# Optimization experiments

Measured on AMD Instinct MI355X. Metric: run time of the kernel, lower is better.

Reference implementation:

```python
import jax, jax.numpy as jnp
import numpy as np

N_DET, N_MAP, N_PTS, C = 900, 100, 20, 256
IMG_W, IMG_H = 640.0, 480.0


def _grid_sample(feat, gx, gy):
    """Bilinear grid_sample, align_corners=False, zeros padding.
    feat: [C,H,W]; gx,gy: [N] normalized in [-1,1]. Returns [N,C]."""
    Cc, H, W = feat.shape
    x = (gx + 1.0) * (W * 0.5) - 0.5
    y = (gy + 1.0) * (H * 0.5) - 0.5
    x0 = jnp.floor(x); y0 = jnp.floor(y)
    wx1 = x - x0; wx0 = 1.0 - wx1
    wy1 = y - y0; wy0 = 1.0 - wy1

    def gather(xi, yi):
        inb = (xi >= 0) & (xi <= W - 1) & (yi >= 0) & (yi <= H - 1)
        xc = jnp.clip(xi, 0, W - 1).astype(jnp.int32)
        yc = jnp.clip(yi, 0, H - 1).astype(jnp.int32)
        return feat[:, yc, xc] * inb.astype(feat.dtype)  # [C,N]

    out = (gather(x0, y0) * (wx0 * wy0) + gather(x0 + 1, y0) * (wx1 * wy0)
           + gather(x0, y0 + 1) * (wx0 * wy1) + gather(x0 + 1, y0 + 1) * (wx1 * wy1))
    return out.T  # [N,C]


def _project(E, K, homo):
    """E:[6,4,4], K:[6,3,3], homo:[N,4] -> gx,gy,valid each [6,N]."""
    pc = jnp.einsum('cij,nj->cni', E, homo)            # [6,N,4]
    p2d = jnp.einsum('cij,cnj->cni', K, pc[..., :3])   # [6,N,3]
    depth = p2d[..., 2]
    u = p2d[..., 0] / (depth + 1e-6)
    v = p2d[..., 1] / (depth + 1e-6)
    valid = depth > 0.1
    gx = u / IMG_W * 2.0 - 1.0
    gy = v / IMG_H * 2.0 - 1.0
    return gx, gy, valid


def _sample_multiscale(feats, gx, gy, valid):
    """feats: list of [6,C,H,W]; gx,gy,valid: [6,N] -> [6,N,C]."""
    acc = None
    for f in feats:  # fixed 4 FPN levels
        s = jax.vmap(_grid_sample)(f, gx, gy)  # [6,N,C]
        acc = s if acc is None else acc + s
    acc = acc / len(feats)
    return acc * valid[..., None].astype(acc.dtype)


def setup_inputs():
    key = jax.random.key(0)
    ks = jax.random.split(key, 16)
    f = lambda i, shape, s=1.0: jax.random.normal(ks[i], shape, jnp.float32) * s
    p2 = f(0, (6, C, 120, 160))
    p3 = f(1, (6, C, 60, 80))
    p4 = f(2, (6, C, 30, 40))
    p5 = f(3, (6, C, 15, 20))
    K0 = jnp.array([[500.0, 0.0, 320.0], [0.0, 500.0, 240.0], [0.0, 0.0, 1.0]], jnp.float32)
    intrinsics = jnp.tile(K0, (6, 1, 1)) + f(4, (6, 3, 3), 0.5)
    extrinsics = jnp.tile(jnp.eye(4, dtype=jnp.float32), (6, 1, 1)) + f(5, (6, 4, 4), 0.3)
    det_anchors_3d = f(6, (N_DET, 3), 20.0)
    det_anchors_full = f(7, (N_DET, 11))
    map_anchors = f(8, (N_MAP, N_PTS, 2), 20.0)
    s = 1.0 / float(np.sqrt(C))
    return {
        'p2': p2, 'p3': p3, 'p4': p4, 'p5': p5,
        'intrinsics': intrinsics, 'extrinsics': extrinsics,
        'det_anchors_3d': det_anchors_3d, 'det_anchors_full': det_anchors_full,
        'map_anchors': map_anchors,
        'W1d': f(9, (C, C), s), 'b1d': jnp.zeros((C,), jnp.float32),
        'Wcd': f(10, (C, 4), s), 'bcd': jnp.zeros((4,), jnp.float32),
        'Wod': f(11, (C, 11), s), 'bod': jnp.zeros((11,), jnp.float32),
        'W1m': f(12, (C, C), s), 'b1m': jnp.zeros((C,), jnp.float32),
        'Wcm': f(13, (C, 3), s), 'bcm': jnp.zeros((3,), jnp.float32),
        'Wom': f(14, (C, N_PTS * 2), s), 'bom': jnp.zeros((N_PTS * 2,), jnp.float32),
    }


def reference(p2, p3, p4, p5, intrinsics, extrinsics, det_anchors_3d,
              det_anchors_full, map_anchors, W1d, b1d, Wcd, bcd, Wod, bod,
              W1m, b1m, Wcm, bcm, Wom, bom):
    feats = [p2, p3, p4, p5]
    ones_det = jnp.ones((N_DET, 1), det_anchors_3d.dtype)
    homo_det = jnp.concatenate([det_anchors_3d, ones_det], axis=-1)  # [900,4]
    centers = map_anchors.mean(axis=1)  # [100,2]
    homo_map = jnp.concatenate([centers,
                                jnp.zeros((N_MAP, 1), centers.dtype),
                                jnp.ones((N_MAP, 1), centers.dtype)], axis=-1)  # [100,4]

    gxd, gyd, vd = _project(extrinsics, intrinsics, homo_det)
    det_agg = _sample_multiscale(feats, gxd, gyd, vd).sum(0) / 6.0  # [900,256]
    gxm, gym, vm = _project(extrinsics, intrinsics, homo_map)
    map_agg = _sample_multiscale(feats, gxm, gym, vm).sum(0) / 6.0  # [100,256]

    hd = jax.nn.relu(det_agg @ W1d + b1d)
    det_classes = hd @ Wcd + bcd                     # [900,4]
    det_boxes = det_anchors_full + hd @ Wod + bod    # [900,11]
    hm = jax.nn.relu(map_agg @ W1m + b1m)
    map_classes = hm @ Wcm + bcm                     # [100,3]
    map_lines = map_anchors + (hm @ Wom + bom).reshape(N_MAP, N_PTS, 2)
    return det_classes, det_boxes, map_classes, map_lines
```

## Files before the change

### kernel.cpp

```cpp
#include <hip/hip_runtime.h>

#define CDIM 256
#define NDET 900
#define NMAP 100
#define NPTS 20
#define NBLK (NDET + NMAP)

using u16 = unsigned short;

#define U4OFF 7372800
#define U5OFF 9216000
#define UEND  9676800
#define ACCF  4838400
#define C3STR 1228800
#define C4STR 307200
#define C5STR 76800

__device__ __forceinline__ u16 f2bf(float f) {
    union { float f; unsigned int i; } v; v.f = f;
    return (u16)((v.i + 0x7FFFu + ((v.i >> 16) & 1u)) >> 16);
}
__device__ __forceinline__ float bf2f(u16 u) {
    union { unsigned int i; float f; } v; v.i = ((unsigned int)u) << 16; return v.f;
}

__global__ __launch_bounds__(256, 4) void k1_pack_p2(
    const float* __restrict__ p2, const float* __restrict__ p3,
    const float* __restrict__ p4, const float* __restrict__ p5,
    const float* __restrict__ Kin, const float* __restrict__ Ein,
    const float* __restrict__ det3d, const float* __restrict__ mapanch,
    u16* __restrict__ wsb, float* __restrict__ accw)
{
    const int b = blockIdx.x;
    const int t = threadIdx.x;

    __shared__ float s_tile[64][65];

    if (b < 1800) {
        const int cam = b / 300;
        const int rem = b % 300;
        const int pxT = rem >> 2, chT = rem & 3;
        const int lane = t & 63, wv = t >> 6;
        #pragma unroll
        for (int cc = 0; cc < 16; ++cc) {
            const int chl = wv * 16 + cc;
            s_tile[chl][lane] = p3[(cam * CDIM + chT * 64 + chl) * 4800 + pxT * 64 + lane];
        }
        __syncthreads();
        #pragma unroll
        for (int pp = 0; pp < 16; ++pp) {
            const int pxl = wv * 16 + pp;
            wsb[(cam * 4800 + pxT * 64 + pxl) * CDIM + chT * 64 + lane] = f2bf(s_tile[lane][pxl]);
        }
        return;
    }
    if (b < 1980) {
        const int id = b - 1800;
        const int cam = id / 30, h = id % 30;
        const float4* __restrict__ src = (const float4*)(p4 + ((cam * CDIM + t) * 30 + h) * 40);
        u16* __restrict__ dst = wsb + U4OFF + ((cam * 30 + h) * 40) * CDIM + t;
        #pragma unroll
        for (int w4 = 0; w4 < 10; ++w4) {
            const float4 v = src[w4];
            dst[(w4 * 4 + 0) * CDIM] = f2bf(v.x);
            dst[(w4 * 4 + 1) * CDIM] = f2bf(v.y);
            dst[(w4 * 4 + 2) * CDIM] = f2bf(v.z);
            dst[(w4 * 4 + 3) * CDIM] = f2bf(v.w);
        }
        return;
    }
    if (b < 2070) {
        const int id = b - 1980;
        const int cam = id / 15, h = id % 15;
        const float4* __restrict__ src = (const float4*)(p5 + ((cam * CDIM + t) * 15 + h) * 20);
        u16* __restrict__ dst = wsb + U5OFF + ((cam * 15 + h) * 20) * CDIM + t;
        #pragma unroll
        for (int w4 = 0; w4 < 5; ++w4) {
            const float4 v = src[w4];
            dst[(w4 * 4 + 0) * CDIM] = f2bf(v.x);
            dst[(w4 * 4 + 1) * CDIM] = f2bf(v.y);
            dst[(w4 * 4 + 2) * CDIM] = f2bf(v.z);
            dst[(w4 * 4 + 3) * CDIM] = f2bf(v.w);
        }
        return;
    }

    const int pt = b - 2070;
    const bool isDet = (pt < NDET);
    const int m = pt - NDET;

    __shared__ int   s_off0[7][4];
    __shared__ float s_w0[7][4];
    __shared__ int   s_list0[8];
    __shared__ int   s_n0;

    if (t < 7) {
        float h0, h1, h2;
        if (isDet) {
            h0 = det3d[pt * 3 + 0];
            h1 = det3d[pt * 3 + 1];
            h2 = det3d[pt * 3 + 2];
        } else {
            float cx = 0.f, cy = 0.f;
            #pragma unroll
            for (int j = 0; j < NPTS; ++j) {
                cx += mapanch[(m * NPTS + j) * 2 + 0];
                cy += mapanch[(m * NPTS + j) * 2 + 1];
            }
            h0 = cx / (float)NPTS; h1 = cy / (float)NPTS; h2 = 0.f;
        }
        bool pred = false;
        if (t < 6) {
            const int cam = t;
            float pc[3];
            #pragma unroll
            for (int i = 0; i < 3; ++i) {
                pc[i] = Ein[cam * 16 + i * 4 + 0] * h0
                      + Ein[cam * 16 + i * 4 + 1] * h1
                      + Ein[cam * 16 + i * 4 + 2] * h2
                      + Ein[cam * 16 + i * 4 + 3] * 1.f;
            }
            const float q0 = Kin[cam*9+0]*pc[0] + Kin[cam*9+1]*pc[1] + Kin[cam*9+2]*pc[2];
            const float q1 = Kin[cam*9+3]*pc[0] + Kin[cam*9+4]*pc[1] + Kin[cam*9+5]*pc[2];
            const float q2 = Kin[cam*9+6]*pc[0] + Kin[cam*9+7]*pc[1] + Kin[cam*9+8]*pc[2];
            const float depth = q2;
            const float u = q0 / (depth + 1e-6f);
            const float v = q1 / (depth + 1e-6f);
            const bool valid = (depth > 0.1f);
            const float gx = u / 640.0f * 2.0f - 1.0f;
            const float gy = v / 480.0f * 2.0f - 1.0f;
            const int H = 120, W = 160;
            const float x = (gx + 1.f) * (W * 0.5f) - 0.5f;
            const float y = (gy + 1.f) * (H * 0.5f) - 0.5f;
            const float x0f = floorf(x), y0f = floorf(y);
            const float wx1 = x - x0f, wx0 = 1.f - wx1;
            const float wy1 = y - y0f, wy0 = 1.f - wy1;
            const float x1f = x0f + 1.f, y1f = y0f + 1.f;
            const bool bx0 = (x0f >= 0.f) && (x0f <= (float)(W - 1));
            const bool bx1 = (x1f >= 0.f) && (x1f <= (float)(W - 1));
            const bool by0 = (y0f >= 0.f) && (y0f <= (float)(H - 1));
            const bool by1 = (y1f >= 0.f) && (y1f <= (float)(H - 1));
            const int xc0 = (int)fminf(fmaxf(x0f, 0.f), (float)(W - 1));
            const int xc1 = (int)fminf(fmaxf(x1f, 0.f), (float)(W - 1));
            const int yc0 = (int)fminf(fmaxf(y0f, 0.f), (float)(H - 1));
            const int yc1 = (int)fminf(fmaxf(y1f, 0.f), (float)(H - 1));
            const int base = cam * CDIM * H * W;
            s_off0[t][0] = base + yc0 * W + xc0;
            s_off0[t][1] = base + yc0 * W + xc1;
            s_off0[t][2] = base + yc1 * W + xc0;
            s_off0[t][3] = base + yc1 * W + xc1;
            const float w0 = (bx0 && by0) ? wx0 * wy0 : 0.f;
            const float w1 = (bx1 && by0) ? wx1 * wy0 : 0.f;
            const float w2 = (bx0 && by1) ? wx0 * wy1 : 0.f;
            const float w3 = (bx1 && by1) ? wx1 * wy1 : 0.f;
            s_w0[t][0] = w0; s_w0[t][1] = w1; s_w0[t][2] = w2; s_w0[t][3] = w3;
            pred = valid && ((w0 + w1 + w2 + w3) != 0.f);
        } else {
            s_off0[6][0] = 0; s_off0[6][1] = 0; s_off0[6][2] = 0; s_off0[6][3] = 0;
            s_w0[6][0] = 0.f; s_w0[6][1] = 0.f; s_w0[6][2] = 0.f; s_w0[6][3] = 0.f;
        }
        const unsigned long long mask = __ballot(pred);
        const int n = __popcll(mask);
        const int rank = __popcll(mask & ((1ull << t) - 1ull));
        if (pred) s_list0[rank] = t;
        const int npad = (n + 1) & ~1;
        if (t < 2 && (n + t) < npad) s_list0[n + t] = 6;
        if (t == 0) s_n0 = npad;
    }
    __syncthreads();

    float acc = 0.f;
    const int npad = s_n0;
    const int cHW = t * 19200;
    for (int base = 0; base < npad; base += 2) {
        float v[2][4];
        int tj[2];
        #pragma unroll
        for (int j = 0; j < 2; ++j) {
            const int tt = s_list0[base + j];
            tj[j] = tt;
            v[j][0] = p2[s_off0[tt][0] + cHW];
            v[j][1] = p2[s_off0[tt][1] + cHW];
            v[j][2] = p2[s_off0[tt][2] + cHW];
            v[j][3] = p2[s_off0[tt][3] + cHW];
        }
        #pragma unroll
        for (int j = 0; j < 2; ++j) {
            const int tt = tj[j];
            acc += s_w0[tt][0] * v[j][0] + s_w0[tt][1] * v[j][1]
                 + s_w0[tt][2] * v[j][2] + s_w0[tt][3] * v[j][3];
        }
    }
    accw[pt * CDIM + t] = acc;
}

__global__ __launch_bounds__(256, 4) void k2_gather_mlp(
    const u16* __restrict__ wsb, const float* __restrict__ accw,
    const float* __restrict__ Kin, const float* __restrict__ Ein,
    const float* __restrict__ det3d, const float* __restrict__ detfull,
    const float* __restrict__ mapanch,
    const float* __restrict__ W1d, const float* __restrict__ b1d,
    const float* __restrict__ Wcd, const float* __restrict__ bcd,
    const float* __restrict__ Wod, const float* __restrict__ bod,
    const float* __restrict__ W1m, const float* __restrict__ b1m,
    const float* __restrict__ Wcm, const float* __restrict__ bcm,
    const float* __restrict__ Wom, const float* __restrict__ bom,
    float* __restrict__ out)
{
    const int pt = blockIdx.x;
    const int t  = threadIdx.x;
    const bool isDet = (pt < NDET);
    const int m = pt - NDET;

    __shared__ int   s_off[19][4];
    __shared__ float s_w[19][4];
    __shared__ int   s_list[24];
    __shared__ int   s_n;
    __shared__ float s_vec[CDIM];
    __shared__ float s_hid[CDIM];

    float acc = accw[pt * CDIM + t];

    if (t < 19) {
        float h0, h1, h2;
        if (isDet) {
            h0 = det3d[pt * 3 + 0];
            h1 = det3d[pt * 3 + 1];
            h2 = det3d[pt * 3 + 2];
        } else {
            float cx = 0.f, cy = 0.f;
            #pragma unroll
            for (int j = 0; j < NPTS; ++j) {
                cx += mapanch[(m * NPTS + j) * 2 + 0];
                cy += mapanch[(m * NPTS + j) * 2 + 1];
            }
            h0 = cx / (float)NPTS; h1 = cy / (float)NPTS; h2 = 0.f;
        }
        bool pred = false;
        if (t < 18) {
            const int cam = t / 3, l = 1 + (t % 3);
            float pc[3];
            #pragma unroll
            for (int i = 0; i < 3; ++i) {
                pc[i] = Ein[cam * 16 + i * 4 + 0] * h0
                      + Ein[cam * 16 + i * 4 + 1] * h1
                      + Ein[cam * 16 + i * 4 + 2] * h2
                      + Ein[cam * 16 + i * 4 + 3] * 1.f;
            }
            const float q0 = Kin[cam*9+0]*pc[0] + Kin[cam*9+1]*pc[1] + Kin[cam*9+2]*pc[2];
            const float q1 = Kin[cam*9+3]*pc[0] + Kin[cam*9+4]*pc[1] + Kin[cam*9+5]*pc[2];
            const float q2 = Kin[cam*9+6]*pc[0] + Kin[cam*9+7]*pc[1] + Kin[cam*9+8]*pc[2];
            const float depth = q2;
            const float u = q0 / (depth + 1e-6f);
            const float v = q1 / (depth + 1e-6f);
            const bool valid = (depth > 0.1f);
            const float gx = u / 640.0f * 2.0f - 1.0f;
            const float gy = v / 480.0f * 2.0f - 1.0f;
            const int Hs[4] = {120, 60, 30, 15};
            const int Ws[4] = {160, 80, 40, 20};
            const int H = Hs[l], W = Ws[l];
            const float x = (gx + 1.f) * (W * 0.5f) - 0.5f;
            const float y = (gy + 1.f) * (H * 0.5f) - 0.5f;
            const float x0f = floorf(x), y0f = floorf(y);
            const float wx1 = x - x0f, wx0 = 1.f - wx1;
            const float wy1 = y - y0f, wy0 = 1.f - wy1;
            const float x1f = x0f + 1.f, y1f = y0f + 1.f;
            const bool bx0 = (x0f >= 0.f) && (x0f <= (float)(W - 1));
            const bool bx1 = (x1f >= 0.f) && (x1f <= (float)(W - 1));
            const bool by0 = (y0f >= 0.f) && (y0f <= (float)(H - 1));
            const bool by1 = (y1f >= 0.f) && (y1f <= (float)(H - 1));
            const int xc0 = (int)fminf(fmaxf(x0f, 0.f), (float)(W - 1));
            const int xc1 = (int)fminf(fmaxf(x1f, 0.f), (float)(W - 1));
            const int yc0 = (int)fminf(fmaxf(y0f, 0.f), (float)(H - 1));
            const int yc1 = (int)fminf(fmaxf(y1f, 0.f), (float)(H - 1));
            const int pb = (l == 1) ? cam * C3STR
                         : (l == 2) ? (U4OFF + cam * C4STR)
                                    : (U5OFF + cam * C5STR);
            s_off[t][0] = pb + (yc0 * W + xc0) * CDIM;
            s_off[t][1] = pb + (yc0 * W + xc1) * CDIM;
            s_off[t][2] = pb + (yc1 * W + xc0) * CDIM;
            s_off[t][3] = pb + (yc1 * W + xc1) * CDIM;
            const float w0 = (bx0 && by0) ? wx0 * wy0 : 0.f;
            const float w1 = (bx1 && by0) ? wx1 * wy0 : 0.f;
            const float w2 = (bx0 && by1) ? wx0 * wy1 : 0.f;
            const float w3 = (bx1 && by1) ? wx1 * wy1 : 0.f;
            s_w[t][0] = w0; s_w[t][1] = w1; s_w[t][2] = w2; s_w[t][3] = w3;
            pred = valid && ((w0 + w1 + w2 + w3) != 0.f);
        } else {
            s_off[18][0] = 0; s_off[18][1] = 0; s_off[18][2] = 0; s_off[18][3] = 0;
            s_w[18][0] = 0.f; s_w[18][1] = 0.f; s_w[18][2] = 0.f; s_w[18][3] = 0.f;
        }
        const unsigned long long mask = __ballot(pred);
        const int n = __popcll(mask);
        const int rank = __popcll(mask & ((1ull << t) - 1ull));
        if (pred) s_list[rank] = t;
        const int npad = (n + 7) & ~7;
        if (t < 8 && (n + t) < npad) s_list[n + t] = 18;
        if (t == 0) s_n = npad;
    }
    __syncthreads();

    const int npad = s_n;
    for (int base = 0; base < npad; base += 8) {
        float v[8][4];
        int tj[8];
        #pragma unroll
        for (int j = 0; j < 8; ++j) {
            const int tt = s_list[base + j];
            tj[j] = tt;
            v[j][0] = bf2f(wsb[s_off[tt][0] + t]);
            v[j][1] = bf2f(wsb[s_off[tt][1] + t]);
            v[j][2] = bf2f(wsb[s_off[tt][2] + t]);
            v[j][3] = bf2f(wsb[s_off[tt][3] + t]);
        }
        #pragma unroll
        for (int j = 0; j < 8; ++j) {
            const int tt = tj[j];
            acc += s_w[tt][0] * v[j][0] + s_w[tt][1] * v[j][1]
                 + s_w[tt][2] * v[j][2] + s_w[tt][3] * v[j][3];
        }
    }
    const float agg = (acc * 0.25f) / 6.0f;

    s_vec[t] = agg;
    __syncthreads();

    const float* __restrict__ W1 = isDet ? W1d : W1m;
    const float* __restrict__ b1 = isDet ? b1d : b1m;
    float hsum = b1[t];
    const float4* sv4 = (const float4*)s_vec;
    float wvA[32], wvB[32];
    #pragma unroll
    for (int i = 0; i < 32; ++i) wvA[i] = W1[i * CDIM + t];
    #pragma unroll
    for (int k0 = 0; k0 < CDIM; k0 += 64) {
        #pragma unroll
        for (int i = 0; i < 32; ++i) wvB[i] = W1[(k0 + 32 + i) * CDIM + t];
        #pragma unroll
        for (int i = 0; i < 8; ++i) {
            const float4 x = sv4[(k0 >> 2) + i];
            hsum = fmaf(x.x, wvA[4 * i + 0], hsum);
            hsum = fmaf(x.y, wvA[4 * i + 1], hsum);
            hsum = fmaf(x.z, wvA[4 * i + 2], hsum);
            hsum = fmaf(x.w, wvA[4 * i + 3], hsum);
        }
        if (k0 + 64 < CDIM) {
            #pragma unroll
            for (int i = 0; i < 32; ++i) wvA[i] = W1[(k0 + 64 + i) * CDIM + t];
        }
        #pragma unroll
        for (int i = 0; i < 8; ++i) {
            const float4 x = sv4[(k0 >> 2) + 8 + i];
            hsum = fmaf(x.x, wvB[4 * i + 0], hsum);
            hsum = fmaf(x.y, wvB[4 * i + 1], hsum);
            hsum = fmaf(x.z, wvB[4 * i + 2], hsum);
            hsum = fmaf(x.w, wvB[4 * i + 3], hsum);
        }
    }
    s_hid[t] = fmaxf(hsum, 0.f);
    __syncthreads();

    const int g  = t >> 4;
    const int ln = t & 15;
    const int nOut = isDet ? 15 : 43;
    const int nrep = isDet ? 1 : 3;
    for (int rep = 0; rep < nrep; ++rep) {
        const int o = g + rep * 16;
        if (o < nOut) {
            const float* Wp; int stride, oo, ooff; float bias;
            if (isDet) {
                if (o < 4) { Wp = Wcd; stride = 4;  oo = o;     ooff = pt * 4 + oo;         bias = bcd[oo]; }
                else       { Wp = Wod; stride = 11; oo = o - 4; ooff = 3600 + pt * 11 + oo; bias = bod[oo] + detfull[pt * 11 + oo]; }
            } else {
                if (o < 3) { Wp = Wcm; stride = 3;  oo = o;     ooff = 13500 + m * 3 + oo;  bias = bcm[oo]; }
                else       { Wp = Wom; stride = 40; oo = o - 3; ooff = 13800 + m * 40 + oo; bias = bom[oo] + mapanch[m * 40 + oo]; }
            }
            float wv[16], xv[16];
            #pragma unroll
            for (int kk = 0; kk < 16; ++kk) wv[kk] = Wp[(ln + kk * 16) * stride + oo];
            #pragma unroll
            for (int kk = 0; kk < 16; ++kk) xv[kk] = s_hid[ln + kk * 16];
            float sp = 0.f;
            #pragma unroll
            for (int kk = 0; kk < 16; ++kk) sp = fmaf(xv[kk], wv[kk], sp);
            #pragma unroll
            for (int off = 1; off < 16; off <<= 1) sp += __shfl_xor(sp, off, 64);
            if (ln == 0) out[ooff] = sp + bias;
        }
    }
}

extern "C" void kernel_launch(void* const* d_in, const int* in_sizes, int n_in,
                              void* d_out, int out_size, void* d_ws, size_t ws_size,
                              hipStream_t stream) {
    const float* p2      = (const float*)d_in[0];
    const float* p3      = (const float*)d_in[1];
    const float* p4      = (const float*)d_in[2];
    const float* p5      = (const float*)d_in[3];
    const float* Kin     = (const float*)d_in[4];
    const float* Ein     = (const float*)d_in[5];
    const float* det3d   = (const float*)d_in[6];
    const float* detfull = (const float*)d_in[7];
    const float* mapanch = (const float*)d_in[8];
    const float* W1d     = (const float*)d_in[9];
    const float* b1d     = (const float*)d_in[10];
    const float* Wcd     = (const float*)d_in[11];
    const float* bcd     = (const float*)d_in[12];
    const float* Wod     = (const float*)d_in[13];
    const float* bod     = (const float*)d_in[14];
    const float* W1m     = (const float*)d_in[15];
    const float* b1m     = (const float*)d_in[16];
    const float* Wcm     = (const float*)d_in[17];
    const float* bcm     = (const float*)d_in[18];
    const float* Wom     = (const float*)d_in[19];
    const float* bom     = (const float*)d_in[20];
    float* out = (float*)d_out;
    u16* wsb = (u16*)d_ws;
    float* accw = (float*)d_ws + ACCF;

    k1_pack_p2<<<3070, 256, 0, stream>>>(
        p2, p3, p4, p5, Kin, Ein, det3d, mapanch, wsb, accw);

    k2_gather_mlp<<<NBLK, 256, 0, stream>>>(
        wsb, accw, Kin, Ein, det3d, detfull, mapanch,
        W1d, b1d, Wcd, bcd, Wod, bod, W1m, b1m, Wcm, bcm, Wom, bom, out);
}
```

Measured before the change: 51.02 us.

## Split p2 level sampling into one block per camera-point pair

```diff
diff --git a/kernel.cpp b/kernel.cpp
--- a/kernel.cpp
+++ b/kernel.cpp
@@ -10,8 +10,7 @@
 
 #define U4OFF 7372800
 #define U5OFF 9216000
-#define UEND  9676800
-#define ACCF  4838400
+#define ACC6F 4838400
 #define C3STR 1228800
 #define C4STR 307200
 #define C5STR 76800
@@ -29,7 +28,7 @@
     const float* __restrict__ p4, const float* __restrict__ p5,
     const float* __restrict__ Kin, const float* __restrict__ Ein,
     const float* __restrict__ det3d, const float* __restrict__ mapanch,
-    u16* __restrict__ wsb, float* __restrict__ accw)
+    u16* __restrict__ wsb, float* __restrict__ acc6)
 {
     const int b = blockIdx.x;
     const int t = threadIdx.x;
@@ -85,117 +84,77 @@
         return;
     }
 
-    const int pt = b - 2070;
+    const int id = b - 2070;
+    const int cam = id / 1000;
+    const int pt = id % 1000;
     const bool isDet = (pt < NDET);
     const int m = pt - NDET;
 
-    __shared__ int   s_off0[7][4];
-    __shared__ float s_w0[7][4];
-    __shared__ int   s_list0[8];
-    __shared__ int   s_n0;
-
-    if (t < 7) {
-        float h0, h1, h2;
-        if (isDet) {
-            h0 = det3d[pt * 3 + 0];
-            h1 = det3d[pt * 3 + 1];
-            h2 = det3d[pt * 3 + 2];
-        } else {
-            float cx = 0.f, cy = 0.f;
-            #pragma unroll
-            for (int j = 0; j < NPTS; ++j) {
-                cx += mapanch[(m * NPTS + j) * 2 + 0];
-                cy += mapanch[(m * NPTS + j) * 2 + 1];
-            }
-            h0 = cx / (float)NPTS; h1 = cy / (float)NPTS; h2 = 0.f;
-        }
-        bool pred = false;
-        if (t < 6) {
-            const int cam = t;
-            float pc[3];
-            #pragma unroll
-            for (int i = 0; i < 3; ++i) {
-                pc[i] = Ein[cam * 16 + i * 4 + 0] * h0
-                      + Ein[cam * 16 + i * 4 + 1] * h1
-                      + Ein[cam * 16 + i * 4 + 2] * h2
-                      + Ein[cam * 16 + i * 4 + 3] * 1.f;
-            }
-            const float q0 = Kin[cam*9+0]*pc[0] + Kin[cam*9+1]*pc[1] + Kin[cam*9+2]*pc[2];
-            const float q1 = Kin[cam*9+3]*pc[0] + Kin[cam*9+4]*pc[1] + Kin[cam*9+5]*pc[2];
-            const float q2 = Kin[cam*9+6]*pc[0] + Kin[cam*9+7]*pc[1] + Kin[cam*9+8]*pc[2];
-            const float depth = q2;
-            const float u = q0 / (depth + 1e-6f);
-            const float v = q1 / (depth + 1e-6f);
-            const bool valid = (depth > 0.1f);
-            const float gx = u / 640.0f * 2.0f - 1.0f;
-            const float gy = v / 480.0f * 2.0f - 1.0f;
-            const int H = 120, W = 160;
-            const float x = (gx + 1.f) * (W * 0.5f) - 0.5f;
-            const float y = (gy + 1.f) * (H * 0.5f) - 0.5f;
-            const float x0f = floorf(x), y0f = floorf(y);
-            const float wx1 = x - x0f, wx0 = 1.f - wx1;
-            const float wy1 = y - y0f, wy0 = 1.f - wy1;
-            const float x1f = x0f + 1.f, y1f = y0f + 1.f;
-            const bool bx0 = (x0f >= 0.f) && (x0f <= (float)(W - 1));
-            const bool bx1 = (x1f >= 0.f) && (x1f <= (float)(W - 1));
-            const bool by0 = (y0f >= 0.f) && (y0f <= (float)(H - 1));
-            const bool by1 = (y1f >= 0.f) && (y1f <= (float)(H - 1));
-            const int xc0 = (int)fminf(fmaxf(x0f, 0.f), (float)(W - 1));
-            const int xc1 = (int)fminf(fmaxf(x1f, 0.f), (float)(W - 1));
-            const int yc0 = (int)fminf(fmaxf(y0f, 0.f), (float)(H - 1));
-            const int yc1 = (int)fminf(fmaxf(y1f, 0.f), (float)(H - 1));
-            const int base = cam * CDIM * H * W;
-            s_off0[t][0] = base + yc0 * W + xc0;
-            s_off0[t][1] = base + yc0 * W + xc1;
-            s_off0[t][2] = base + yc1 * W + xc0;
-            s_off0[t][3] = base + yc1 * W + xc1;
-            const float w0 = (bx0 && by0) ? wx0 * wy0 : 0.f;
-            const float w1 = (bx1 && by0) ? wx1 * wy0 : 0.f;
-            const float w2 = (bx0 && by1) ? wx0 * wy1 : 0.f;
-            const float w3 = (bx1 && by1) ? wx1 * wy1 : 0.f;
-            s_w0[t][0] = w0; s_w0[t][1] = w1; s_w0[t][2] = w2; s_w0[t][3] = w3;
-            pred = valid && ((w0 + w1 + w2 + w3) != 0.f);
-        } else {
-            s_off0[6][0] = 0; s_off0[6][1] = 0; s_off0[6][2] = 0; s_off0[6][3] = 0;
-            s_w0[6][0] = 0.f; s_w0[6][1] = 0.f; s_w0[6][2] = 0.f; s_w0[6][3] = 0.f;
-        }
-        const unsigned long long mask = __ballot(pred);
-        const int n = __popcll(mask);
-        const int rank = __popcll(mask & ((1ull << t) - 1ull));
-        if (pred) s_list0[rank] = t;
-        const int npad = (n + 1) & ~1;
-        if (t < 2 && (n + t) < npad) s_list0[n + t] = 6;
-        if (t == 0) s_n0 = npad;
-    }
-    __syncthreads();
-
-    float acc = 0.f;
-    const int npad = s_n0;
-    const int cHW = t * 19200;
-    for (int base = 0; base < npad; base += 2) {
-        float v[2][4];
-        int tj[2];
-        #pragma unroll
-        for (int j = 0; j < 2; ++j) {
-            const int tt = s_list0[base + j];
-            tj[j] = tt;
-            v[j][0] = p2[s_off0[tt][0] + cHW];
-            v[j][1] = p2[s_off0[tt][1] + cHW];
-            v[j][2] = p2[s_off0[tt][2] + cHW];
-            v[j][3] = p2[s_off0[tt][3] + cHW];
-        }
-        #pragma unroll
-        for (int j = 0; j < 2; ++j) {
-            const int tt = tj[j];
-            acc += s_w0[tt][0] * v[j][0] + s_w0[tt][1] * v[j][1]
-                 + s_w0[tt][2] * v[j][2] + s_w0[tt][3] * v[j][3];
-        }
-    }
-    accw[pt * CDIM + t] = acc;
+    float h0, h1, h2;
+    if (isDet) {
+        h0 = det3d[pt * 3 + 0];
+        h1 = det3d[pt * 3 + 1];
+        h2 = det3d[pt * 3 + 2];
+    } else {
+        float cx = 0.f, cy = 0.f;
+        #pragma unroll
+        for (int j = 0; j < NPTS; ++j) {
+            cx += mapanch[(m * NPTS + j) * 2 + 0];
+            cy += mapanch[(m * NPTS + j) * 2 + 1];
+        }
+        h0 = cx / (float)NPTS; h1 = cy / (float)NPTS; h2 = 0.f;
+    }
+    float pc[3];
+    #pragma unroll
+    for (int i = 0; i < 3; ++i) {
+        pc[i] = Ein[cam * 16 + i * 4 + 0] * h0
+              + Ein[cam * 16 + i * 4 + 1] * h1
+              + Ein[cam * 16 + i * 4 + 2] * h2
+              + Ein[cam * 16 + i * 4 + 3] * 1.f;
+    }
+    const float q0 = Kin[cam*9+0]*pc[0] + Kin[cam*9+1]*pc[1] + Kin[cam*9+2]*pc[2];
+    const float q1 = Kin[cam*9+3]*pc[0] + Kin[cam*9+4]*pc[1] + Kin[cam*9+5]*pc[2];
+    const float q2 = Kin[cam*9+6]*pc[0] + Kin[cam*9+7]*pc[1] + Kin[cam*9+8]*pc[2];
+    const float depth = q2;
+    const float u = q0 / (depth + 1e-6f);
+    const float v = q1 / (depth + 1e-6f);
+    const bool valid = (depth > 0.1f);
+    const float gx = u / 640.0f * 2.0f - 1.0f;
+    const float gy = v / 480.0f * 2.0f - 1.0f;
+    const int H = 120, W = 160;
+    const float x = (gx + 1.f) * (W * 0.5f) - 0.5f;
+    const float y = (gy + 1.f) * (H * 0.5f) - 0.5f;
+    const float x0f = floorf(x), y0f = floorf(y);
+    const float wx1 = x - x0f, wx0 = 1.f - wx1;
+    const float wy1 = y - y0f, wy0 = 1.f - wy1;
+    const float x1f = x0f + 1.f, y1f = y0f + 1.f;
+    const bool bx0 = (x0f >= 0.f) && (x0f <= (float)(W - 1));
+    const bool bx1 = (x1f >= 0.f) && (x1f <= (float)(W - 1));
+    const bool by0 = (y0f >= 0.f) && (y0f <= (float)(H - 1));
+    const bool by1 = (y1f >= 0.f) && (y1f <= (float)(H - 1));
+    const int xc0 = (int)fminf(fmaxf(x0f, 0.f), (float)(W - 1));
+    const int xc1 = (int)fminf(fmaxf(x1f, 0.f), (float)(W - 1));
+    const int yc0 = (int)fminf(fmaxf(y0f, 0.f), (float)(H - 1));
+    const int yc1 = (int)fminf(fmaxf(y1f, 0.f), (float)(H - 1));
+    const float w0 = (bx0 && by0) ? wx0 * wy0 : 0.f;
+    const float w1 = (bx1 && by0) ? wx1 * wy0 : 0.f;
+    const float w2 = (bx0 && by1) ? wx0 * wy1 : 0.f;
+    const float w3 = (bx1 && by1) ? wx1 * wy1 : 0.f;
+
+    float res = 0.f;
+    if (valid && ((w0 + w1 + w2 + w3) != 0.f)) {
+        const int base = cam * CDIM * H * W + t * (H * W);
+        const float v0 = p2[base + yc0 * W + xc0];
+        const float v1 = p2[base + yc0 * W + xc1];
+        const float v2 = p2[base + yc1 * W + xc0];
+        const float v3 = p2[base + yc1 * W + xc1];
+        res = w0 * v0 + w1 * v1 + w2 * v2 + w3 * v3;
+    }
+    acc6[(cam * 1000 + pt) * CDIM + t] = res;
 }
 
 __global__ __launch_bounds__(256, 4) void k2_gather_mlp(
-    const u16* __restrict__ wsb, const float* __restrict__ accw,
+    const u16* __restrict__ wsb, const float* __restrict__ acc6,
     const float* __restrict__ Kin, const float* __restrict__ Ein,
     const float* __restrict__ det3d, const float* __restrict__ detfull,
     const float* __restrict__ mapanch,
@@ -219,7 +178,13 @@
     __shared__ float s_vec[CDIM];
     __shared__ float s_hid[CDIM];
 
-    float acc = accw[pt * CDIM + t];
+    float a0 = acc6[(0 * 1000 + pt) * CDIM + t];
+    float a1 = acc6[(1 * 1000 + pt) * CDIM + t];
+    float a2 = acc6[(2 * 1000 + pt) * CDIM + t];
+    float a3 = acc6[(3 * 1000 + pt) * CDIM + t];
+    float a4 = acc6[(4 * 1000 + pt) * CDIM + t];
+    float a5 = acc6[(5 * 1000 + pt) * CDIM + t];
+    float acc = ((((a0 + a1) + a2) + a3) + a4) + a5;
 
     if (t < 19) {
         float h0, h1, h2;
@@ -416,12 +381,12 @@
     const float* bom     = (const float*)d_in[20];
     float* out = (float*)d_out;
     u16* wsb = (u16*)d_ws;
-    float* accw = (float*)d_ws + ACCF;
-
-    k1_pack_p2<<<3070, 256, 0, stream>>>(
-        p2, p3, p4, p5, Kin, Ein, det3d, mapanch, wsb, accw);
+    float* acc6 = (float*)d_ws + ACC6F;
+
+    k1_pack_p2<<<8070, 256, 0, stream>>>(
+        p2, p3, p4, p5, Kin, Ein, det3d, mapanch, wsb, acc6);
 
     k2_gather_mlp<<<NBLK, 256, 0, stream>>>(
-        wsb, accw, Kin, Ein, det3d, detfull, mapanch,
+        wsb, acc6, Kin, Ein, det3d, detfull, mapanch,
         W1d, b1d, Wcd, bcd, Wod, bod, W1m, b1m, Wcm, bcm, Wom, bom, out);
 }
```

Measured after the change: 44.54 us. 12.7% less time.
